# Kernel optimization log

Measured on AMD Instinct MI355X. Metric: run time of the kernel, lower is better.

The kernel has to match this reference:

```python
import jax, jax.numpy as jnp
import numpy as np

L, B, S, D, H = 6, 2, 2048, 512, 8
DH = D // H
FF = 4 * D
EPS = 1e-5


def setup_inputs() -> dict:
    key = jax.random.key(0)
    ks = jax.random.split(key, 10)
    w = lambda k, shape: jax.random.normal(k, shape, jnp.float32) * 0.02
    return {
        "query": jax.random.normal(ks[0], (B, S, D), jnp.float32),
        "key": jax.random.normal(ks[1], (B, S, D), jnp.float32),
        "query_mask": jnp.ones((B, S), jnp.int32),
        "key_mask": jnp.ones((B, S), jnp.int32),
        # per-layer stacked params; conv1d(kernel=1) == linear with weight [out,in]
        "Wq": w(ks[2], (L, D, D)), "bq": jnp.zeros((L, D), jnp.float32),
        "Wk": w(ks[3], (L, D, D)), "bk": jnp.zeros((L, D), jnp.float32),
        "Wv": w(ks[4], (L, D, D)), "bv": jnp.zeros((L, D), jnp.float32),
        "Wo": w(ks[5], (L, D, D)), "bo": jnp.zeros((L, D), jnp.float32),
        "ln1_g": jnp.ones((L, D), jnp.float32), "ln1_b": jnp.zeros((L, D), jnp.float32),
        "ff_w1": w(ks[6], (L, FF, D)), "ff_b1": jnp.zeros((L, FF), jnp.float32),
        "ff_w2": w(ks[7], (L, D, FF)), "ff_b2": jnp.zeros((L, D), jnp.float32),
        "ln2_g": jnp.ones((L, D), jnp.float32), "ln2_b": jnp.zeros((L, D), jnp.float32),
    }


def _layer_norm(x, g, b):
    m = jnp.mean(x, axis=-1, keepdims=True)
    v = jnp.mean(jnp.square(x - m), axis=-1, keepdims=True)
    return (x - m) * jax.lax.rsqrt(v + EPS) * g + b


def reference(query, key, query_mask, key_mask,
              Wq, bq, Wk, bk, Wv, bv, Wo, bo,
              ln1_g, ln1_b, ff_w1, ff_b1, ff_w2, ff_b2, ln2_g, ln2_b):
    b_, s_, d_ = query.shape
    kpad = (key_mask == 0)[:, None, None, :]          # [B,1,1,K]
    qm = query_mask.astype(query.dtype)[:, :, None]    # [B,S,1]
    x = query
    for i in range(L):
        # QKV projections (conv1d kernel-size-1 == linear), split heads -> [B,H,S,DH]
        def split(t):
            return t.reshape(b_, s_, H, DH).transpose(0, 2, 1, 3)
        q = split(x @ Wq[i].T + bq[i]) * (float(DH) ** -0.5)
        k = split(key @ Wk[i].T + bk[i])
        v = split(key @ Wv[i].T + bv[i])
        attn = jnp.einsum('bhqd,bhkd->bhqk', q, k)
        attn = jnp.where(kpad, -jnp.inf, attn)
        attn = jax.nn.softmax(attn, axis=-1)
        o = jnp.einsum('bhqk,bhkd->bhqd', attn, v)
        o = o.transpose(0, 2, 1, 3).reshape(b_, s_, H * DH)
        o = (o @ Wo[i].T + bo[i]) * qm                 # output proj + query mask
        x = _layer_norm(o + x, ln1_g[i], ln1_b[i])
        h = jax.nn.leaky_relu(x @ ff_w1[i].T + ff_b1[i], 0.01)
        f = (h @ ff_w2[i].T + ff_b2[i]) * qm           # FFN mask on output
        x = _layer_norm(f + x, ln2_g[i], ln2_b[i])
    return x
```

## Files before the change

### kernel.cpp

```cpp
#include <hip/hip_runtime.h>
#include <stdint.h>

constexpr int LAYERS = 6;
constexpr int Bc = 2, Sc = 2048, Dc = 512, Hc = 8, DHc = 64, FFc = 2048;
constexpr int Mc = Bc * Sc;
constexpr int NS = 2;
constexpr int KCHUNK = Sc / NS;

typedef __attribute__((ext_vector_type(8))) __bf16 bf16x8;
typedef __attribute__((ext_vector_type(4))) __bf16 bf16x4;
typedef __attribute__((ext_vector_type(4))) float f32x4;

__device__ __forceinline__ void async_ld16(const void* g, void* lds) {
  __builtin_amdgcn_global_load_lds(
      (const __attribute__((address_space(1))) uint32_t*)g,
      (__attribute__((address_space(3))) uint32_t*)lds, 16, 0, 0);
}

__global__ __launch_bounds__(256) void cvt_kernel(const float* __restrict__ in,
                                                  __bf16* __restrict__ out, int n) {
  int i = (blockIdx.x * 256 + threadIdx.x) * 4;
  if (i + 4 > n) return;
  const float4 v = *(const float4*)(in + i);
  bf16x4 o;
  o[0] = (__bf16)v.x; o[1] = (__bf16)v.y; o[2] = (__bf16)v.z; o[3] = (__bf16)v.w;
  *(bf16x4*)(out + i) = o;
}

__global__ __launch_bounds__(256) void cvt_kv_kernel(const float* __restrict__ Wk,
                                                     const float* __restrict__ Wv,
                                                     __bf16* __restrict__ out) {
  size_t i = ((size_t)blockIdx.x * 256 + threadIdx.x) * 4;
  int n = (int)(i / ((size_t)Dc * Dc));
  int lyr = n >> 1, p = n & 1;
  size_t idx = i - (size_t)n * Dc * Dc;
  const float* src = (p ? Wv : Wk) + (size_t)lyr * Dc * Dc + idx;
  const float4 v = *(const float4*)src;
  bf16x4 o;
  o[0] = (__bf16)v.x; o[1] = (__bf16)v.y; o[2] = (__bf16)v.z; o[3] = (__bf16)v.w;
  *(bf16x4*)(out + i) = o;
}

__global__ __launch_bounds__(256) void kbias_kernel(const int* __restrict__ km,
                                                    float* __restrict__ kb, int n) {
  int i = blockIdx.x * 256 + threadIdx.x;
  if (i < n) kb[i] = km[i] ? 0.f : -1e30f;
}

template <int BM, int BN, int WM, int WN, int EPI>
__global__ __launch_bounds__(256) void gemm_bt(
    const __bf16* __restrict__ A, const __bf16* __restrict__ W,
    const float* __restrict__ bias, const float* __restrict__ bias2,
    float* __restrict__ outf, __bf16* __restrict__ outb,
    __bf16* __restrict__ outb2, float scale,
    int M, int N, int K, int Kstride) {
  constexpr int BK = 64;
  __shared__ __bf16 As[2][BM * BK];
  __shared__ __bf16 Bs[2][BN * BK];
  const int tid = threadIdx.x;
  const int l15 = tid & 15;
  const int lg = (tid & 63) >> 4;
  const int w = tid >> 6;
  const int wm = w >> 1, wn = w & 1;
  const int tm = blockIdx.y * BM;
  const int tn = blockIdx.x * BN;
  const int z = blockIdx.z;
  const __bf16* Ap = A + (size_t)tm * Kstride + (size_t)z * K;
  const __bf16* Wp = W + (size_t)tn * Kstride + (size_t)z * K;
  f32x4 acc[WM][WN] = {};

  auto stage = [&](int k0, int bf) {
#pragma unroll
    for (int c = 0; c < BM * 8 / 256; ++c) {
      int cc = c * 256 + tid;
      int r = cc >> 3, s = cc & 7;
      int ss = s ^ (r & 7);
      async_ld16(Ap + (size_t)r * Kstride + k0 + ss * 8, &As[bf][cc * 8]);
    }
#pragma unroll
    for (int c = 0; c < BN * 8 / 256; ++c) {
      int cc = c * 256 + tid;
      int r = cc >> 3, s = cc & 7;
      int ss = s ^ (r & 7);
      async_ld16(Wp + (size_t)r * Kstride + k0 + ss * 8, &Bs[bf][cc * 8]);
    }
  };

  const int nk = K / BK;
  stage(0, 0);
  __syncthreads();
  int buf = 0;
  for (int t = 0; t < nk; ++t) {
    if (t + 1 < nk) stage((t + 1) * BK, buf ^ 1);
    bf16x8 af[WM][2], bfr[WN][2];
#pragma unroll
    for (int i = 0; i < WM; ++i) {
      int row = wm * WM * 16 + i * 16 + l15;
#pragma unroll
      for (int kf = 0; kf < 2; ++kf)
        af[i][kf] = *(const bf16x8*)&As[buf][row * 64 + (((kf * 4 + lg) ^ (row & 7)) * 8)];
    }
#pragma unroll
    for (int j = 0; j < WN; ++j) {
      int row = wn * WN * 16 + j * 16 + l15;
#pragma unroll
      for (int kf = 0; kf < 2; ++kf)
        bfr[j][kf] = *(const bf16x8*)&Bs[buf][row * 64 + (((kf * 4 + lg) ^ (row & 7)) * 8)];
    }
#pragma unroll
    for (int kf = 0; kf < 2; ++kf)
#pragma unroll
      for (int i = 0; i < WM; ++i)
#pragma unroll
        for (int j = 0; j < WN; ++j)
          acc[i][j] = __builtin_amdgcn_mfma_f32_16x16x32_bf16(af[i][kf], bfr[j][kf], acc[i][j], 0, 0, 0);
    __syncthreads();
    buf ^= 1;
  }

  if constexpr (EPI == 6) {
    const bool isV = ((tn & 1023) >= 512);
    const int lyr = tn >> 10;
    const int b = tm >> 11;
    const int sbase = tm & (Sc - 1);
    if (isV) {
      __bf16* T = (__bf16*)&As[0][0];
#pragma unroll
      for (int i = 0; i < WM; ++i) {
#pragma unroll
        for (int j = 0; j < WN; ++j) {
          const int d = wn * WN * 16 + j * 16 + l15;
          const int dg = (tn & 511) + d;
          const float bv = bias2[lyr * 512 + dg];
          const int s0 = wm * WM * 16 + i * 16 + lg * 4;
          bf16x4 pk;
#pragma unroll
          for (int r = 0; r < 4; ++r) pk[r] = (__bf16)(acc[i][j][r] + bv);
          const int slot = (s0 >> 3) ^ (d & 7);
          *(bf16x4*)&T[d * 64 + slot * 8 + (s0 & 7)] = pk;
        }
      }
      __syncthreads();
      const int rr = tid >> 3;
      const int c8 = tid & 7;
#pragma unroll
      for (int pass = 0; pass < 4; ++pass) {
        const int d = pass * 32 + rr;
        const int slot = c8 ^ (d & 7);
        bf16x8 v8 = *(const bf16x8*)&T[d * 64 + slot * 8];
        const int dg = (tn & 511) + d;
        const int h = dg >> 6, dh = dg & 63;
        *(bf16x8*)&outb2[((((size_t)(lyr * Bc + b) * Hc + h)) * DHc + dh) * Sc +
                         sbase + c8 * 8] = v8;
      }
    } else {
#pragma unroll
      for (int i = 0; i < WM; ++i) {
#pragma unroll
        for (int j = 0; j < WN; ++j) {
          const int d = wn * WN * 16 + j * 16 + l15;
          const int dg = (tn & 511) + d;
          const float bv = bias[lyr * 512 + dg];
          const int h = dg >> 6, dh = dg & 63;
#pragma unroll
          for (int r = 0; r < 4; ++r) {
            const int s = sbase + wm * WM * 16 + i * 16 + lg * 4 + r;
            outb[((((size_t)(lyr * Bc + b) * Hc + h)) * Sc + s) * DHc + dh] =
                (__bf16)(acc[i][j][r] + bv);
          }
        }
      }
    }
    return;
  }

#pragma unroll
  for (int i = 0; i < WM; ++i) {
#pragma unroll
    for (int j = 0; j < WN; ++j) {
      const int n = tn + wn * WN * 16 + j * 16 + l15;
      float bv;
      if constexpr (EPI == 0) {
        bv = (z == 0) ? bias[n] : 0.f;
      } else {
        bv = bias[n];
      }
#pragma unroll
      for (int r = 0; r < 4; ++r) {
        const int m = tm + wm * WM * 16 + i * 16 + lg * 4 + r;
        float v = acc[i][j][r] + bv;
        if constexpr (EPI == 0) {
          outf[(size_t)z * M * N + (size_t)m * N + n] = v;
        } else if constexpr (EPI == 1) {
          int b = m >> 11, s = m & (Sc - 1);
          int h = n >> 6, dh = n & 63;
          outb[(((size_t)(b * Hc + h)) * Sc + s) * DHc + dh] = (__bf16)(v * scale);
        } else if constexpr (EPI == 4) {
          float lv = v > 0.f ? v : 0.01f * v;
          outb[(size_t)m * N + n] = (__bf16)lv;
        }
      }
    }
  }
}

__global__ __launch_bounds__(256, 5) void attn_kernel(
    const __bf16* __restrict__ q, const __bf16* __restrict__ k,
    const __bf16* __restrict__ vt, const float* __restrict__ kb,
    __bf16* __restrict__ Opart, float* __restrict__ mpart,
    float* __restrict__ lpart) {
  const int bid = blockIdx.x;
  const int o = (bid & 7) * 128 + (bid >> 3);
  const int qb = o & 31;
  const int p = o >> 5;
  const int bh = p >> 1;
  const int z = p & 1;
  const int b = bh >> 3;
  const int w = threadIdx.x >> 6;
  const int l = threadIdx.x & 63;
  const int l15 = l & 15;
  const int lg = l >> 4;
  const int tid = threadIdx.x;
  const int qbase = qb * 64 + w * 16;
  const int k0 = z * KCHUNK;

  const __bf16* qp = q + ((size_t)bh * Sc + qbase) * DHc;
  const __bf16* kp = k + (size_t)bh * Sc * DHc;
  const __bf16* vp = vt + (size_t)bh * DHc * Sc;
  const float* kbp = kb + (size_t)b * Sc;

  bf16x8 qf[2];
  qf[0] = *(const bf16x8*)(qp + l15 * DHc + lg * 8);
  qf[1] = *(const bf16x8*)(qp + l15 * DHc + 32 + lg * 8);

  bf16x8 onesf;
#pragma unroll
  for (int i = 0; i < 8; ++i) onesf[i] = (__bf16)1.0f;

  f32x4 oacc[4] = {};
  f32x4 lacc = {};
  float mr = -1e30f;

  __shared__ __bf16 Ks[2][4096];
  __shared__ __bf16 Vs[2][4096];

  auto stage = [&](int t, int bf) {
    const int kt = k0 + t * 64;
#pragma unroll
    for (int ii = 0; ii < 2; ++ii) {
      int i = ii * 256 + tid;
      int r = i >> 3;
      int bsrc = (i & 7) ^ (r & 7);
      async_ld16(kp + (size_t)(kt + r) * DHc + bsrc * 8, &Ks[bf][i * 8]);
      async_ld16(vp + (size_t)r * Sc + kt + bsrc * 8, &Vs[bf][i * 8]);
    }
  };

  stage(0, 0);
  __syncthreads();

  constexpr int NT = KCHUNK / 64;
  int buf = 0;
  for (int t = 0; t < NT; ++t) {
    const int kt = k0 + t * 64;
    if (t + 1 < NT) stage(t + 1, buf ^ 1);

    float4 mb4[4];
#pragma unroll
    for (int cb = 0; cb < 4; ++cb)
      mb4[cb] = *(const float4*)&kbp[kt + cb * 16 + lg * 4];

    f32x4 sacc[4] = {};
#pragma unroll
    for (int kf = 0; kf < 2; ++kf) {
#pragma unroll
      for (int cb = 0; cb < 4; ++cb) {
        int row = cb * 16 + l15;
        bf16x8 kfr = *(const bf16x8*)&Ks[buf][row * 64 + (((kf * 4 + lg) ^ (row & 7)) * 8)];
        sacc[cb] = __builtin_amdgcn_mfma_f32_16x16x32_bf16(kfr, qf[kf], sacc[cb], 0, 0, 0);
      }
    }
    sacc[0][0] += mb4[0].x; sacc[0][1] += mb4[0].y; sacc[0][2] += mb4[0].z; sacc[0][3] += mb4[0].w;
    sacc[1][0] += mb4[1].x; sacc[1][1] += mb4[1].y; sacc[1][2] += mb4[1].z; sacc[1][3] += mb4[1].w;
    sacc[2][0] += mb4[2].x; sacc[2][1] += mb4[2].y; sacc[2][2] += mb4[2].z; sacc[2][3] += mb4[2].w;
    sacc[3][0] += mb4[3].x; sacc[3][1] += mb4[3].y; sacc[3][2] += mb4[3].z; sacc[3][3] += mb4[3].w;

    float mx = sacc[0][0];
#pragma unroll
    for (int cb = 0; cb < 4; ++cb)
#pragma unroll
      for (int r = 0; r < 4; ++r) mx = fmaxf(mx, sacc[cb][r]);
    mx = fmaxf(mx, __shfl_xor(mx, 16, 64));
    mx = fmaxf(mx, __shfl_xor(mx, 32, 64));

    if (__any(mx > mr + 8.f)) {
      float mn = fmaxf(mr, mx);
      float f = __expf(mr - mn);
      mr = mn;
      float fj[4];
#pragma unroll
      for (int j = 0; j < 4; ++j) fj[j] = __shfl(f, lg * 4 + j, 64);
#pragma unroll
      for (int j = 0; j < 4; ++j) lacc[j] *= fj[j];
#pragma unroll
      for (int db = 0; db < 4; ++db)
#pragma unroll
        for (int j = 0; j < 4; ++j) oacc[db][j] *= fj[j];
    }

    unsigned pw[4][2];
#pragma unroll
    for (int cb = 0; cb < 4; ++cb) {
#pragma unroll
      for (int w2 = 0; w2 < 2; ++w2) {
        union { __bf16 h[2]; unsigned u; } cu;
        cu.h[0] = (__bf16)__expf(sacc[cb][2 * w2] - mr);
        cu.h[1] = (__bf16)__expf(sacc[cb][2 * w2 + 1] - mr);
        pw[cb][w2] = cu.u;
      }
    }

    const int srcA = ((lg & 1) * 2) * 16 + l15;
    const int srcB = srcA + 16;
    const bool hi = (lg >> 1) & 1;
#pragma unroll
    for (int kf = 0; kf < 2; ++kf) {
      unsigned t0a = __shfl((int)pw[kf * 2][0], srcA, 64);
      unsigned t0b = __shfl((int)pw[kf * 2 + 1][0], srcA, 64);
      unsigned t1a = __shfl((int)pw[kf * 2][1], srcA, 64);
      unsigned t1b = __shfl((int)pw[kf * 2 + 1][1], srcA, 64);
      unsigned t2a = __shfl((int)pw[kf * 2][0], srcB, 64);
      unsigned t2b = __shfl((int)pw[kf * 2 + 1][0], srcB, 64);
      unsigned t3a = __shfl((int)pw[kf * 2][1], srcB, 64);
      unsigned t3b = __shfl((int)pw[kf * 2 + 1][1], srcB, 64);
      union { unsigned u[4]; bf16x8 v; } pa;
      pa.u[0] = hi ? t0b : t0a;
      pa.u[1] = hi ? t1b : t1a;
      pa.u[2] = hi ? t2b : t2a;
      pa.u[3] = hi ? t3b : t3a;
      lacc = __builtin_amdgcn_mfma_f32_16x16x32_bf16(pa.v, onesf, lacc, 0, 0, 0);
#pragma unroll
      for (int db = 0; db < 4; ++db) {
        int row = db * 16 + l15;
        bf16x8 vf = *(const bf16x8*)&Vs[buf][row * 64 + (((kf * 4 + lg) ^ (row & 7)) * 8)];
        oacc[db] = __builtin_amdgcn_mfma_f32_16x16x32_bf16(pa.v, vf, oacc[db], 0, 0, 0);
      }
    }
    __syncthreads();
    buf ^= 1;
  }

  const size_t obase = (((size_t)(z * Bc * Hc + bh)) * Sc + qbase) * DHc;
#pragma unroll
  for (int db = 0; db < 4; ++db)
#pragma unroll
    for (int j = 0; j < 4; ++j)
      Opart[obase + (size_t)(lg * 4 + j) * DHc + db * 16 + l15] = (__bf16)oacc[db][j];
  const int row0 = (z * Bc * Hc + bh) * Sc + qbase;
  if (lg == 0) mpart[row0 + l15] = mr;
  if (l15 == 0) {
#pragma unroll
    for (int j = 0; j < 4; ++j) lpart[row0 + lg * 4 + j] = lacc[j];
  }
}

__global__ __launch_bounds__(256) void attn_combine(
    const __bf16* __restrict__ Opart, const float* __restrict__ mpart,
    const float* __restrict__ lpart, __bf16* __restrict__ out) {
  int t = blockIdx.x * 256 + threadIdx.x;
  int d = t & 63;
  int row = t >> 6;
  int bh = row >> 11, s = row & (Sc - 1);
  constexpr int RSTRIDE = Bc * Hc * Sc;
  float m0 = mpart[row], m1 = mpart[RSTRIDE + row];
  float l0 = lpart[row], l1 = lpart[RSTRIDE + row];
  float M = fmaxf(m0, m1);
  float e0 = __expf(m0 - M), e1 = __expf(m1 - M);
  float denom = e0 * l0 + e1 * l1;
  float o0 = (float)Opart[(size_t)row * DHc + d];
  float o1 = (float)Opart[((size_t)RSTRIDE + row) * DHc + d];
  float o = (e0 * o0 + e1 * o1) / denom;
  int b = bh >> 3, h = bh & 7;
  out[(((size_t)b * Sc + s)) * Dc + h * DHc + d] = (__bf16)o;
}

__global__ __launch_bounds__(256) void add_ln_kernel(
    const float* __restrict__ res, const float* __restrict__ res2,
    const int* __restrict__ rmask, const float* __restrict__ xin,
    const float* __restrict__ g, const float* __restrict__ bb,
    float* __restrict__ xo, __bf16* __restrict__ xbo) {
  const int row = blockIdx.x;
  const int tid = threadIdx.x;
  const float* rp = res + (size_t)row * Dc;
  const float* xp = xin + (size_t)row * Dc;
  float mfac = rmask ? (float)rmask[row] : 1.f;
  float a0 = rp[tid], a1 = rp[tid + 256];
  if (res2) {
    const float* r2p = res2 + (size_t)row * Dc;
    a0 += r2p[tid];
    a1 += r2p[tid + 256];
  }
  float v0 = a0 * mfac + xp[tid];
  float v1 = a1 * mfac + xp[tid + 256];
  float s = v0 + v1;
#pragma unroll
  for (int d = 1; d < 64; d <<= 1) s += __shfl_xor(s, d, 64);
  __shared__ float red[4], red2[4];
  if ((tid & 63) == 0) red[tid >> 6] = s;
  __syncthreads();
  float mean = (red[0] + red[1] + red[2] + red[3]) * (1.0f / Dc);
  float d0 = v0 - mean, d1 = v1 - mean;
  float qq = d0 * d0 + d1 * d1;
#pragma unroll
  for (int d = 1; d < 64; d <<= 1) qq += __shfl_xor(qq, d, 64);
  if ((tid & 63) == 0) red2[tid >> 6] = qq;
  __syncthreads();
  float var = (red2[0] + red2[1] + red2[2] + red2[3]) * (1.0f / Dc);
  float rs = rsqrtf(var + 1e-5f);
  float o0 = d0 * rs * g[tid] + bb[tid];
  float o1 = d1 * rs * g[tid + 256] + bb[tid + 256];
  xo[(size_t)row * Dc + tid] = o0;
  xo[(size_t)row * Dc + tid + 256] = o1;
  xbo[(size_t)row * Dc + tid] = (__bf16)o0;
  xbo[(size_t)row * Dc + tid + 256] = (__bf16)o1;
}

extern "C" void kernel_launch(void* const* d_in, const int* in_sizes, int n_in,
                              void* d_out, int out_size, void* d_ws, size_t ws_size,
                              hipStream_t stream) {
  (void)in_sizes; (void)n_in; (void)out_size; (void)ws_size;
  const float* query = (const float*)d_in[0];
  const float* key   = (const float*)d_in[1];
  const int* qmask   = (const int*)d_in[2];
  const int* kmask   = (const int*)d_in[3];
  const float* Wq = (const float*)d_in[4];
  const float* bq = (const float*)d_in[5];
  const float* Wk = (const float*)d_in[6];
  const float* bk = (const float*)d_in[7];
  const float* Wv = (const float*)d_in[8];
  const float* bv = (const float*)d_in[9];
  const float* Wo = (const float*)d_in[10];
  const float* bo = (const float*)d_in[11];
  const float* ln1g = (const float*)d_in[12];
  const float* ln1b = (const float*)d_in[13];
  const float* fw1 = (const float*)d_in[14];
  const float* fb1 = (const float*)d_in[15];
  const float* fw2 = (const float*)d_in[16];
  const float* fb2 = (const float*)d_in[17];
  const float* ln2g = (const float*)d_in[18];
  const float* ln2b = (const float*)d_in[19];

  char* ws = (char*)d_ws;
  size_t off = 0;
  auto carve = [&](size_t bytes) -> void* {
    void* p = ws + off;
    off += (bytes + 255) & ~(size_t)255;
    return p;
  };
  float* x_f    = (float*)carve((size_t)Mc * Dc * 4);
  float* tmp_f  = (float*)carve((size_t)2 * Mc * Dc * 4);
  __bf16* x_b   = (__bf16*)carve((size_t)Mc * Dc * 2);
  __bf16* key_b = (__bf16*)carve((size_t)Mc * Dc * 2);
  __bf16* q_b   = (__bf16*)carve((size_t)Mc * Dc * 2);
  __bf16* at_b  = (__bf16*)carve((size_t)Mc * Dc * 2);
  __bf16* h_b   = (__bf16*)carve((size_t)Mc * FFc * 2);
  __bf16* k_all = (__bf16*)carve((size_t)LAYERS * Mc * Dc * 2);
  __bf16* vt_all= (__bf16*)carve((size_t)LAYERS * Mc * Dc * 2);
  __bf16* wq_b  = (__bf16*)carve((size_t)LAYERS * Dc * Dc * 2);
  __bf16* wkv_b = (__bf16*)carve((size_t)LAYERS * 2 * Dc * Dc * 2);
  __bf16* wo_b  = (__bf16*)carve((size_t)LAYERS * Dc * Dc * 2);
  __bf16* w1_b  = (__bf16*)carve((size_t)LAYERS * FFc * Dc * 2);
  __bf16* w2_b  = (__bf16*)carve((size_t)LAYERS * Dc * FFc * 2);
  float* ml_f   = (float*)carve((size_t)NS * Bc * Hc * Sc * 4 * 2);
  float* kb_f   = (float*)carve((size_t)Bc * Sc * 4);

  __bf16* opart_b = h_b;
  float* mpart_f = ml_f;
  float* lpart_f = ml_f + (size_t)NS * Bc * Hc * Sc;
  float* tmp2_f = tmp_f + (size_t)Mc * Dc;

  auto cvt = [&](const float* src, __bf16* dst, int n) {
    cvt_kernel<<<n / 1024, 256, 0, stream>>>(src, dst, n);
  };
  cvt(query, x_b, Mc * Dc);
  cvt(key, key_b, Mc * Dc);
  cvt(Wq, wq_b, LAYERS * Dc * Dc);
  cvt_kv_kernel<<<LAYERS * 2 * Dc * Dc / 1024, 256, 0, stream>>>(Wk, Wv, wkv_b);
  cvt(Wo, wo_b, LAYERS * Dc * Dc);
  cvt(fw1, w1_b, LAYERS * FFc * Dc);
  cvt(fw2, w2_b, LAYERS * Dc * FFc);
  kbias_kernel<<<Bc * Sc / 256, 256, 0, stream>>>(kmask, kb_f, Bc * Sc);
  hipMemcpyAsync(x_f, query, (size_t)Mc * Dc * 4, hipMemcpyDeviceToDevice, stream);

  const dim3 blk(256);
  const dim3 gP64(Dc / 64, Mc / 64);
  const dim3 gOP(Dc / 64, Mc / 64, 2);
  const dim3 gFF2(Dc / 64, Mc / 64, 2);
  const dim3 gKV(LAYERS * 2 * Dc / 128, Mc / 64);
  const dim3 gFF1(FFc / 128, Mc / 64);
  const dim3 gAttn(Sc / 64 * Bc * Hc * NS);
  const dim3 gComb(Bc * Hc * Sc * DHc / 256);

  gemm_bt<64, 128, 2, 4, 6><<<gKV, blk, 0, stream>>>(
      key_b, wkv_b, bk, bv, nullptr, k_all, vt_all, 1.0f,
      Mc, LAYERS * 2 * Dc, Dc, Dc);

  for (int i = 0; i < LAYERS; ++i) {
    const __bf16* wq_i = wq_b + (size_t)i * Dc * Dc;
    const __bf16* wo_i = wo_b + (size_t)i * Dc * Dc;
    const __bf16* w1_i = w1_b + (size_t)i * FFc * Dc;
    const __bf16* w2_i = w2_b + (size_t)i * Dc * FFc;
    const __bf16* k_i  = k_all + (size_t)i * Mc * Dc;
    const __bf16* vt_i = vt_all + (size_t)i * Mc * Dc;

    gemm_bt<64, 64, 2, 2, 1><<<gP64, blk, 0, stream>>>(
        x_b, wq_i, bq + i * Dc, nullptr, nullptr, q_b, nullptr, 0.125f,
        Mc, Dc, Dc, Dc);
    attn_kernel<<<gAttn, blk, 0, stream>>>(q_b, k_i, vt_i, kb_f,
                                           opart_b, mpart_f, lpart_f);
    attn_combine<<<gComb, blk, 0, stream>>>(opart_b, mpart_f, lpart_f, at_b);
    gemm_bt<64, 64, 2, 2, 0><<<gOP, blk, 0, stream>>>(
        at_b, wo_i, bo + i * Dc, nullptr, tmp_f, nullptr, nullptr, 1.0f,
        Mc, Dc, Dc / 2, Dc);
    add_ln_kernel<<<Mc, blk, 0, stream>>>(tmp_f, tmp2_f, qmask, x_f,
                                          ln1g + i * Dc, ln1b + i * Dc, x_f, x_b);
    gemm_bt<64, 128, 2, 4, 4><<<gFF1, blk, 0, stream>>>(
        x_b, w1_i, fb1 + i * FFc, nullptr, nullptr, h_b, nullptr, 1.0f,
        Mc, FFc, Dc, Dc);
    gemm_bt<64, 64, 2, 2, 0><<<gFF2, blk, 0, stream>>>(
        h_b, w2_i, fb2 + i * Dc, nullptr, tmp_f, nullptr, nullptr, 1.0f,
        Mc, Dc, FFc / 2, FFc);
    add_ln_kernel<<<Mc, blk, 0, stream>>>(tmp_f, tmp2_f, qmask, x_f,
                                          ln2g + i * Dc, ln2b + i * Dc, x_f, x_b);
  }
  hipMemcpyAsync(d_out, x_f, (size_t)Mc * Dc * 4, hipMemcpyDeviceToDevice, stream);
}
```

Baseline: 815.4 us.

## Fuse split-K attention combine into output projection GEMM, raise split counts

Removes the separate attention-combine kernel by merging the flash-decoding partial outputs (rescaling with the per-split max and sum) inside the A-tile loader of a new output-projection GEMM. The attention K-split rises from 2 to 4 and the FFN2 split-K from 2 to 4, with add_ln summing a variable number of partial buffers. s_setprio is set around the MFMA blocks in attention. The changes add more partial-output traffic and extra combine arithmetic inside the GEMM, in exchange for one fewer launch and more parallelism per layer.

```diff
diff --git a/kernel.cpp b/kernel.cpp
--- a/kernel.cpp
+++ b/kernel.cpp
@@ -4,7 +4,7 @@
 constexpr int LAYERS = 6;
 constexpr int Bc = 2, Sc = 2048, Dc = 512, Hc = 8, DHc = 64, FFc = 2048;
 constexpr int Mc = Bc * Sc;
-constexpr int NS = 2;
+constexpr int NS = 4;
 constexpr int KCHUNK = Sc / NS;
 
 typedef __attribute__((ext_vector_type(8))) __bf16 bf16x8;
@@ -204,17 +204,138 @@
   }
 }
 
+__global__ __launch_bounds__(256) void gemm_op(
+    const __bf16* __restrict__ Opart, const float* __restrict__ mpart,
+    const float* __restrict__ lpart, const __bf16* __restrict__ W,
+    const float* __restrict__ bias, float* __restrict__ outf) {
+  constexpr int BM = 64, BN = 64;
+  __shared__ __bf16 As[2][BM * 64];
+  __shared__ __bf16 Bs[2][BN * 64];
+  const int tid = threadIdx.x;
+  const int l15 = tid & 15;
+  const int lg = (tid & 63) >> 4;
+  const int w = tid >> 6;
+  const int wm = w >> 1, wn = w & 1;
+  const int tm = blockIdx.y * BM;
+  const int tn = blockIdx.x * BN;
+  const int z = blockIdx.z;
+  const __bf16* Wp = W + (size_t)tn * Dc + z * 256;
+  f32x4 acc[2][2] = {};
+
+  auto stageB = [&](int k0, int bf) {
+#pragma unroll
+    for (int c = 0; c < 2; ++c) {
+      int cc = c * 256 + tid;
+      int r = cc >> 3, s = cc & 7, ss = s ^ (r & 7);
+      async_ld16(Wp + (size_t)r * Dc + k0 + ss * 8, &Bs[bf][cc * 8]);
+    }
+  };
+
+  bf16x8 og[2][NS];
+  float eg[2][NS], invg[2];
+  auto loadA = [&](int t) {
+#pragma unroll
+    for (int c = 0; c < 2; ++c) {
+      int cc = c * 256 + tid;
+      int r = cc >> 3, s = cc & 7, ss = s ^ (r & 7);
+      int mrow = tm + r;
+      int b = mrow >> 11, sq = mrow & (Sc - 1);
+      int bh = b * Hc + (z * 4 + t);
+      int dh0 = ss * 8;
+      float mz[NS], lz[NS];
+      float M = -1e30f;
+#pragma unroll
+      for (int zz = 0; zz < NS; ++zz) {
+        og[c][zz] = *(const bf16x8*)&Opart[(((size_t)(zz * 16 + bh)) * Sc + sq) * DHc + dh0];
+        mz[zz] = mpart[(zz * 16 + bh) * Sc + sq];
+        lz[zz] = lpart[(zz * 16 + bh) * Sc + sq];
+        M = fmaxf(M, mz[zz]);
+      }
+      float den = 0.f;
+#pragma unroll
+      for (int zz = 0; zz < NS; ++zz) {
+        eg[c][zz] = __expf(mz[zz] - M);
+        den += eg[c][zz] * lz[zz];
+      }
+      invg[c] = 1.0f / den;
+    }
+  };
+  auto writeA = [&](int bf) {
+#pragma unroll
+    for (int c = 0; c < 2; ++c) {
+      int cc = c * 256 + tid;
+      bf16x8 cmb;
+#pragma unroll
+      for (int e = 0; e < 8; ++e) {
+        float a = 0.f;
+#pragma unroll
+        for (int zz = 0; zz < NS; ++zz) a += eg[c][zz] * (float)og[c][zz][e];
+        cmb[e] = (__bf16)(a * invg[c]);
+      }
+      *(bf16x8*)&As[bf][cc * 8] = cmb;
+    }
+  };
+
+  loadA(0);
+  stageB(0, 0);
+  writeA(0);
+  __syncthreads();
+  int buf = 0;
+  for (int t = 0; t < 4; ++t) {
+    if (t + 1 < 4) { loadA(t + 1); stageB((t + 1) * 64, buf ^ 1); }
+    bf16x8 af[2][2], bfr[2][2];
+#pragma unroll
+    for (int i = 0; i < 2; ++i) {
+      int row = wm * 32 + i * 16 + l15;
+#pragma unroll
+      for (int kf = 0; kf < 2; ++kf)
+        af[i][kf] = *(const bf16x8*)&As[buf][row * 64 + (((kf * 4 + lg) ^ (row & 7)) * 8)];
+    }
+#pragma unroll
+    for (int j = 0; j < 2; ++j) {
+      int row = wn * 32 + j * 16 + l15;
+#pragma unroll
+      for (int kf = 0; kf < 2; ++kf)
+        bfr[j][kf] = *(const bf16x8*)&Bs[buf][row * 64 + (((kf * 4 + lg) ^ (row & 7)) * 8)];
+    }
+#pragma unroll
+    for (int kf = 0; kf < 2; ++kf)
+#pragma unroll
+      for (int i = 0; i < 2; ++i)
+#pragma unroll
+        for (int j = 0; j < 2; ++j)
+          acc[i][j] = __builtin_amdgcn_mfma_f32_16x16x32_bf16(af[i][kf], bfr[j][kf], acc[i][j], 0, 0, 0);
+    if (t + 1 < 4) writeA(buf ^ 1);
+    __syncthreads();
+    buf ^= 1;
+  }
+
+#pragma unroll
+  for (int i = 0; i < 2; ++i) {
+#pragma unroll
+    for (int j = 0; j < 2; ++j) {
+      const int n = tn + wn * 32 + j * 16 + l15;
+      const float bv = (z == 0) ? bias[n] : 0.f;
+#pragma unroll
+      for (int r = 0; r < 4; ++r) {
+        const int m = tm + wm * 32 + i * 16 + lg * 4 + r;
+        outf[(size_t)z * Mc * Dc + (size_t)m * Dc + n] = acc[i][j][r] + bv;
+      }
+    }
+  }
+}
+
 __global__ __launch_bounds__(256, 5) void attn_kernel(
     const __bf16* __restrict__ q, const __bf16* __restrict__ k,
     const __bf16* __restrict__ vt, const float* __restrict__ kb,
     __bf16* __restrict__ Opart, float* __restrict__ mpart,
     float* __restrict__ lpart) {
   const int bid = blockIdx.x;
-  const int o = (bid & 7) * 128 + (bid >> 3);
+  const int o = (bid & 7) * 256 + (bid >> 3);
   const int qb = o & 31;
   const int p = o >> 5;
-  const int bh = p >> 1;
-  const int z = p & 1;
+  const int bh = p >> 2;
+  const int z = p & 3;
   const int b = bh >> 3;
   const int w = threadIdx.x >> 6;
   const int l = threadIdx.x & 63;
@@ -271,6 +392,7 @@
       mb4[cb] = *(const float4*)&kbp[kt + cb * 16 + lg * 4];
 
     f32x4 sacc[4] = {};
+    __builtin_amdgcn_s_setprio(1);
 #pragma unroll
     for (int kf = 0; kf < 2; ++kf) {
 #pragma unroll
@@ -280,6 +402,7 @@
         sacc[cb] = __builtin_amdgcn_mfma_f32_16x16x32_bf16(kfr, qf[kf], sacc[cb], 0, 0, 0);
       }
     }
+    __builtin_amdgcn_s_setprio(0);
     sacc[0][0] += mb4[0].x; sacc[0][1] += mb4[0].y; sacc[0][2] += mb4[0].z; sacc[0][3] += mb4[0].w;
     sacc[1][0] += mb4[1].x; sacc[1][1] += mb4[1].y; sacc[1][2] += mb4[1].z; sacc[1][3] += mb4[1].w;
     sacc[2][0] += mb4[2].x; sacc[2][1] += mb4[2].y; sacc[2][2] += mb4[2].z; sacc[2][3] += mb4[2].w;
@@ -338,6 +461,7 @@
       pa.u[1] = hi ? t1b : t1a;
       pa.u[2] = hi ? t2b : t2a;
       pa.u[3] = hi ? t3b : t3a;
+      __builtin_amdgcn_s_setprio(1);
       lacc = __builtin_amdgcn_mfma_f32_16x16x32_bf16(pa.v, onesf, lacc, 0, 0, 0);
 #pragma unroll
       for (int db = 0; db < 4; ++db) {
@@ -345,6 +469,7 @@
         bf16x8 vf = *(const bf16x8*)&Vs[buf][row * 64 + (((kf * 4 + lg) ^ (row & 7)) * 8)];
         oacc[db] = __builtin_amdgcn_mfma_f32_16x16x32_bf16(pa.v, vf, oacc[db], 0, 0, 0);
       }
+      __builtin_amdgcn_s_setprio(0);
     }
     __syncthreads();
     buf ^= 1;
@@ -364,41 +489,21 @@
   }
 }
 
-__global__ __launch_bounds__(256) void attn_combine(
-    const __bf16* __restrict__ Opart, const float* __restrict__ mpart,
-    const float* __restrict__ lpart, __bf16* __restrict__ out) {
-  int t = blockIdx.x * 256 + threadIdx.x;
-  int d = t & 63;
-  int row = t >> 6;
-  int bh = row >> 11, s = row & (Sc - 1);
-  constexpr int RSTRIDE = Bc * Hc * Sc;
-  float m0 = mpart[row], m1 = mpart[RSTRIDE + row];
-  float l0 = lpart[row], l1 = lpart[RSTRIDE + row];
-  float M = fmaxf(m0, m1);
-  float e0 = __expf(m0 - M), e1 = __expf(m1 - M);
-  float denom = e0 * l0 + e1 * l1;
-  float o0 = (float)Opart[(size_t)row * DHc + d];
-  float o1 = (float)Opart[((size_t)RSTRIDE + row) * DHc + d];
-  float o = (e0 * o0 + e1 * o1) / denom;
-  int b = bh >> 3, h = bh & 7;
-  out[(((size_t)b * Sc + s)) * Dc + h * DHc + d] = (__bf16)o;
-}
-
 __global__ __launch_bounds__(256) void add_ln_kernel(
-    const float* __restrict__ res, const float* __restrict__ res2,
+    const float* __restrict__ res, int nz,
     const int* __restrict__ rmask, const float* __restrict__ xin,
     const float* __restrict__ g, const float* __restrict__ bb,
     float* __restrict__ xo, __bf16* __restrict__ xbo) {
   const int row = blockIdx.x;
   const int tid = threadIdx.x;
-  const float* rp = res + (size_t)row * Dc;
+  const size_t MD = (size_t)Mc * Dc;
   const float* xp = xin + (size_t)row * Dc;
   float mfac = rmask ? (float)rmask[row] : 1.f;
-  float a0 = rp[tid], a1 = rp[tid + 256];
-  if (res2) {
-    const float* r2p = res2 + (size_t)row * Dc;
-    a0 += r2p[tid];
-    a1 += r2p[tid + 256];
+  float a0 = 0.f, a1 = 0.f;
+  for (int j = 0; j < nz; ++j) {
+    const float* rp = res + j * MD + (size_t)row * Dc;
+    a0 += rp[tid];
+    a1 += rp[tid + 256];
   }
   float v0 = a0 * mfac + xp[tid];
   float v1 = a1 * mfac + xp[tid + 256];
@@ -458,11 +563,10 @@
     return p;
   };
   float* x_f    = (float*)carve((size_t)Mc * Dc * 4);
-  float* tmp_f  = (float*)carve((size_t)2 * Mc * Dc * 4);
+  float* tmp_f  = (float*)carve((size_t)4 * Mc * Dc * 4);
   __bf16* x_b   = (__bf16*)carve((size_t)Mc * Dc * 2);
   __bf16* key_b = (__bf16*)carve((size_t)Mc * Dc * 2);
   __bf16* q_b   = (__bf16*)carve((size_t)Mc * Dc * 2);
-  __bf16* at_b  = (__bf16*)carve((size_t)Mc * Dc * 2);
   __bf16* h_b   = (__bf16*)carve((size_t)Mc * FFc * 2);
   __bf16* k_all = (__bf16*)carve((size_t)LAYERS * Mc * Dc * 2);
   __bf16* vt_all= (__bf16*)carve((size_t)LAYERS * Mc * Dc * 2);
@@ -477,7 +581,6 @@
   __bf16* opart_b = h_b;
   float* mpart_f = ml_f;
   float* lpart_f = ml_f + (size_t)NS * Bc * Hc * Sc;
-  float* tmp2_f = tmp_f + (size_t)Mc * Dc;
 
   auto cvt = [&](const float* src, __bf16* dst, int n) {
     cvt_kernel<<<n / 1024, 256, 0, stream>>>(src, dst, n);
@@ -495,12 +598,10 @@
   const dim3 blk(256);
   const dim3 gP64(Dc / 64, Mc / 64);
   const dim3 gOP(Dc / 64, Mc / 64, 2);
-  const dim3 gFF2(Dc / 64, Mc / 64, 2);
+  const dim3 gFF2(Dc / 64, Mc / 64, 4);
   const dim3 gKV(LAYERS * 2 * Dc / 128, Mc / 64);
   const dim3 gFF1(FFc / 128, Mc / 64);
   const dim3 gAttn(Sc / 64 * Bc * Hc * NS);
-  const dim3 gComb(Bc * Hc * Sc * DHc / 256);
-
   gemm_bt<64, 128, 2, 4, 6><<<gKV, blk, 0, stream>>>(
       key_b, wkv_b, bk, bv, nullptr, k_all, vt_all, 1.0f,
       Mc, LAYERS * 2 * Dc, Dc, Dc);
@@ -518,19 +619,17 @@
         Mc, Dc, Dc, Dc);
     attn_kernel<<<gAttn, blk, 0, stream>>>(q_b, k_i, vt_i, kb_f,
                                            opart_b, mpart_f, lpart_f);
-    attn_combine<<<gComb, blk, 0, stream>>>(opart_b, mpart_f, lpart_f, at_b);
-    gemm_bt<64, 64, 2, 2, 0><<<gOP, blk, 0, stream>>>(
-        at_b, wo_i, bo + i * Dc, nullptr, tmp_f, nullptr, nullptr, 1.0f,
-        Mc, Dc, Dc / 2, Dc);
-    add_ln_kernel<<<Mc, blk, 0, stream>>>(tmp_f, tmp2_f, qmask, x_f,
+    gemm_op<<<gOP, blk, 0, stream>>>(opart_b, mpart_f, lpart_f, wo_i,
+                                     bo + i * Dc, tmp_f);
+    add_ln_kernel<<<Mc, blk, 0, stream>>>(tmp_f, 2, qmask, x_f,
                                           ln1g + i * Dc, ln1b + i * Dc, x_f, x_b);
     gemm_bt<64, 128, 2, 4, 4><<<gFF1, blk, 0, stream>>>(
         x_b, w1_i, fb1 + i * FFc, nullptr, nullptr, h_b, nullptr, 1.0f,
         Mc, FFc, Dc, Dc);
     gemm_bt<64, 64, 2, 2, 0><<<gFF2, blk, 0, stream>>>(
         h_b, w2_i, fb2 + i * Dc, nullptr, tmp_f, nullptr, nullptr, 1.0f,
-        Mc, Dc, FFc / 2, FFc);
-    add_ln_kernel<<<Mc, blk, 0, stream>>>(tmp_f, tmp2_f, qmask, x_f,
+        Mc, Dc, FFc / 4, FFc);
+    add_ln_kernel<<<Mc, blk, 0, stream>>>(tmp_f, 4, qmask, x_f,
                                           ln2g + i * Dc, ln2b + i * Dc, x_f, x_b);
   }
   hipMemcpyAsync(d_out, x_f, (size_t)Mc * Dc * 4, hipMemcpyDeviceToDevice, stream);
```

Result: slower. 930.2 us (+14.1%).
